# Optimization experiments

Measured on AMD Instinct MI355X. Metric: run time of the kernel, lower is better.

## Reference

```python
import jax, jax.numpy as jnp
import numpy as np
from jax import lax

N, CIN, H, W = 32, 128, 64, 64
COUT, KH, KW = 256, 3, 3
STRIDE = (1, 1)
PADDING = ((1, 1), (1, 1))


def setup_inputs() -> dict:
    key = jax.random.key(0)
    k1, k2, k3, k4 = jax.random.split(key, 4)
    # binary input in {0,1}
    x = jax.random.randint(k1, (N, CIN, H, W), 0, 2).astype(jnp.float32)
    # ternary weight in {-1,0,1}
    weight = (jax.random.randint(k2, (COUT, CIN, KH, KW), 0, 3) - 1).astype(jnp.float32)
    # integer bias (folded from BN, floored to int per get_sign_bias_from_bn)
    bias = jax.random.randint(k3, (COUT,), -200, 200).astype(jnp.float32)
    # sign in {-1,+1}, broadcast shape (1, COUT, 1, 1)
    sign = jnp.where(jax.random.bernoulli(k4, 0.5, (1, COUT, 1, 1)), 1.0, -1.0).astype(jnp.float32)
    return {"x": x, "weight": weight, "bias": bias, "sign": sign}


def reference(x, weight, bias, sign):
    # y = conv2d(x, W) + bias  (stride 1, pad 1, NCHW)
    y = lax.conv_general_dilated(
        x, weight,
        window_strides=STRIDE,
        padding=PADDING,
        dimension_numbers=("NCHW", "OIHW", "NCHW"),
    ) + bias[None, :, None, None]
    # rounding=True -> torch.round_(y)
    y = jnp.round(y)
    # output = 1 iff sign * y >= 0, cast back to input dtype
    return jnp.where(y * sign >= 0, jnp.float32(1), jnp.float32(0)).astype(x.dtype)
```

## Files before the change

### kernel.cpp

```cpp
#include <hip/hip_runtime.h>
#include <cstdint>


#define NIMG 32
#define CIN  128
#define HH   64
#define WW   64
#define COUT 256
#define X4ROW   4224
#define STG_SY  4352
#define STG_BYTES (4 * STG_SY)
#define LDS_TOTAL (STG_BYTES + 4 * X4ROW)
#define WQ4_BYTES ((size_t)9 * 8 * 2 * 64 * 16)

typedef int   v4i  __attribute__((ext_vector_type(4)));
typedef int   v8i  __attribute__((ext_vector_type(8)));
typedef float v16f __attribute__((ext_vector_type(16)));

__global__ __launch_bounds__(256) void w_prepack(const float* __restrict__ w,
                                                 int8_t* __restrict__ wq4) {
    const int idx = blockIdx.x * 256 + threadIdx.x;
    if (idx >= (int)WQ4_BYTES) return;
    const int b    = idx & 15;
    const int lane = (idx >> 4) & 63;
    const int s    = (idx >> 10) & 1;
    const int co32 = (idx >> 11) & 7;
    const int tap  = idx >> 14;
    const int co   = co32 * 32 + (lane & 31);
    const int ci0  = s * 64 + (lane >> 5) * 32 + b * 2;
    const int i0 = (int)w[(size_t)(co * CIN + ci0) * 9 + tap];
    const int i1 = (int)w[(size_t)(co * CIN + ci0 + 1) * 9 + tap];
    const uint32_t n0 = (i0 == 0) ? 0u : ((i0 > 0) ? 0x2u : 0xAu);
    const uint32_t n1 = (i1 == 0) ? 0u : ((i1 > 0) ? 0x2u : 0xAu);
    wq4[idx] = (int8_t)(n0 | (n1 << 4));
}

__device__ __forceinline__ v8i widen(v4i x) {
    v8i r = {x[0], x[1], x[2], x[3], 0, 0, 0, 0};
    return r;
}

__global__ __launch_bounds__(512) void binconv_fused(
    const float* __restrict__ x, const int8_t* __restrict__ wq4,
    const float* __restrict__ bias, const float* __restrict__ sign,
    float* __restrict__ out) {

    __shared__ __align__(16) int8_t Smem[LDS_TOTAL];
    int8_t* Stg = Smem;
    int8_t* X4  = Smem + STG_BYTES;

    const int t  = threadIdx.x;
    const int bx = blockIdx.x;
    const int n  = bx >> 5;
    const int y0 = (bx & 31) << 1;

    if (t < 256) {
        const int sy = t >> 6;
        const int pr = t & 63;
        const int y  = y0 + sy - 1;
        uint32_t* sp = (uint32_t*)(Stg + sy * STG_SY + pr * 68);
        if (y >= 0 && y < HH) {
            const uint4* r0 =
                (const uint4*)(x + (((size_t)n * CIN + 2 * pr)     * HH + y) * WW);
            const uint4* r1 =
                (const uint4*)(x + (((size_t)n * CIN + 2 * pr + 1) * HH + y) * WW);
#pragma unroll
            for (int q = 0; q < 16; ++q) {
                const uint4 a = r0[q], b = r1[q];
                uint32_t wd = ((a.x >> 28) & 0x2u)        | ((b.x >> 24) & 0x20u)
                            | ((a.y >> 20) & 0x200u)      | ((b.y >> 16) & 0x2000u)
                            | ((a.z >> 12) & 0x20000u)    | ((b.z >> 8) & 0x200000u)
                            | ((a.w >> 4)  & 0x2000000u)  | ( b.w       & 0x20000000u);
                sp[q] = wd;
            }
        } else {
#pragma unroll
            for (int q = 0; q < 16; ++q) sp[q] = 0u;
        }
    }
    __syncthreads();

    if (t < 264) {
        const int sy  = t / 66;
        const int pxp = t - sy * 66;
        int8_t* dst = X4 + sy * X4ROW + pxp * 64;
        if (pxp == 0 || pxp == 65) {
            const int4 z = {0, 0, 0, 0};
#pragma unroll
            for (int c = 0; c < 4; ++c) *(int4*)(dst + c * 16) = z;
        } else {
            const int8_t* src = Stg + sy * STG_SY + (pxp - 1);
            uint32_t wrd[16];
#pragma unroll
            for (int k = 0; k < 16; ++k) {
                const uint32_t b0 = (uint8_t)src[(4 * k + 0) * 68];
                const uint32_t b1 = (uint8_t)src[(4 * k + 1) * 68];
                const uint32_t b2 = (uint8_t)src[(4 * k + 2) * 68];
                const uint32_t b3 = (uint8_t)src[(4 * k + 3) * 68];
                wrd[k] = b0 | (b1 << 8) | (b2 << 16) | (b3 << 24);
            }
            const int sk = pxp & 3;
#pragma unroll
            for (int c = 0; c < 4; ++c) {
                int4 vv = {(int)wrd[c*4], (int)wrd[c*4+1],
                           (int)wrd[c*4+2], (int)wrd[c*4+3]};
                *(int4*)(dst + ((c ^ sk) << 4)) = vv;
            }
        }
    }
    __syncthreads();

    const int wid  = t >> 6;
    const int lane = t & 63;
    const int m_lo = lane & 31;
    const int hi   = lane >> 5;
    const int co_off = (wid >> 1) * 64;
    const int yw     = wid & 1;
    const int ct0    = co_off >> 5;

    const int8_t* Xw  = X4 + yw * X4ROW;
    const int8_t* wqb = wq4 + lane * 16;

    v16f acc[2][2] = {};

#pragma unroll
    for (int tap = 0; tap < 9; ++tap) {
        const int ky = tap / 3, kx = tap % 3;
        const int8_t* xl = Xw + ky * X4ROW;
        const int px0 = m_lo + kx;
        const int pk  = px0 & 3;

        v4i af[2][2];
#pragma unroll
        for (int c = 0; c < 2; ++c)
#pragma unroll
            for (int s = 0; s < 2; ++s)
                af[c][s] = *(const v4i*)(wqb
                    + ((((tap * 8 + ct0 + c) * 2) + s) << 10));

        v4i bf[2][2];
#pragma unroll
        for (int s = 0; s < 2; ++s) {
            const int sw = (((s << 1) + hi) ^ pk) << 4;
#pragma unroll
            for (int m = 0; m < 2; ++m)
                bf[m][s] = *(const v4i*)(xl + (px0 + m * 32) * 64 + sw);
        }
#pragma unroll
        for (int s = 0; s < 2; ++s)
#pragma unroll
            for (int c = 0; c < 2; ++c)
#pragma unroll
                for (int m = 0; m < 2; ++m)
                    acc[c][m] = __builtin_amdgcn_mfma_scale_f32_32x32x64_f8f6f4(
                        widen(af[c][s]), widen(bf[m][s]), acc[c][m],
                        4, 4,
                        0, 0x7F7F7F7F,
                        0, 0x7F7F7F7F);
    }

    const float* bco = bias + co_off;
    const float* sco = sign + co_off;
    float* outb = out + ((size_t)n * COUT + co_off) * (HH * WW)
                + (y0 + yw) * WW + m_lo;
#pragma unroll
    for (int c = 0; c < 2; ++c) {
#pragma unroll
        for (int r = 0; r < 16; ++r) {
            const int co_l = c * 32 + (r & 3) + 8 * (r >> 2) + 4 * hi;
            const float bv = bco[co_l];
            const float sv = sco[co_l];
            float* orow = outb + (size_t)co_l * (HH * WW);
#pragma unroll
            for (int m = 0; m < 2; ++m) {
                const float yv = acc[c][m][r] + bv;
                const bool on = (sv > 0.0f) ? (yv >= 0.0f) : (yv <= 0.0f);
                __builtin_nontemporal_store(on ? 1.0f : 0.0f, orow + m * 32);
            }
        }
    }
}

__global__ __launch_bounds__(256) void naive_conv(
    const float* __restrict__ x, const float* __restrict__ w,
    const float* __restrict__ bias, const float* __restrict__ sign,
    float* __restrict__ out) {
    const int idx = blockIdx.x * 256 + threadIdx.x;
    const int xc = idx & 63, y = (idx >> 6) & 63, co = (idx >> 12) & 255,
              n = idx >> 20;
    float s = 0.f;
    for (int ci = 0; ci < CIN; ++ci)
        for (int ky = 0; ky < 3; ++ky) {
            const int iy = y + ky - 1;
            if (iy < 0 || iy >= HH) continue;
            for (int kx = 0; kx < 3; ++kx) {
                const int ix = xc + kx - 1;
                if (ix < 0 || ix >= WW) continue;
                s += x[((size_t)(n * CIN + ci) * HH + iy) * WW + ix] *
                     w[((size_t)(co * CIN + ci) * 3 + ky) * 3 + kx];
            }
        }
    const float yv = s + bias[co];
    out[idx] = ((sign[co] > 0.f) ? (yv >= 0.f) : (yv <= 0.f)) ? 1.0f : 0.0f;
}

extern "C" void kernel_launch(void* const* d_in, const int* in_sizes, int n_in,
                              void* d_out, int out_size, void* d_ws, size_t ws_size,
                              hipStream_t stream) {
    const float* x    = (const float*)d_in[0];
    const float* w    = (const float*)d_in[1];
    const float* bias = (const float*)d_in[2];
    const float* sign = (const float*)d_in[3];
    float* out = (float*)d_out;

    if (ws_size < WQ4_BYTES) {
        naive_conv<<<dim3((NIMG * COUT * HH * WW) / 256), 256, 0, stream>>>(
            x, w, bias, sign, out);
        return;
    }
    int8_t* wq4 = (int8_t*)d_ws;

    w_prepack<<<dim3((int)((WQ4_BYTES + 255) / 256)), 256, 0, stream>>>(w, wq4);
    binconv_fused<<<dim3(NIMG * (HH / 2)), 512, 0, stream>>>(
        x, wq4, bias, sign, out);
}
```

Before: 206.2 us.

## Spread input staging over all threads, byte-transpose via perm, swizzle block order

The global-load stage now uses all 512 threads, each handling half a row, instead of 256 threads each doing a full row. The LDS byte transpose into the swizzled X4 layout now reads 32-bit words and uses v_perm byte shuffles instead of per-byte LDS reads, with a separate set of threads zeroing the pad columns. Block indices are remapped so that consecutive blocks interleave across images, which may change L2 locality and scheduling. The aim is to cut prologue latency in LDS and VALU before the MFMA loop. The risk is that the perm selectors or the 17-word stride indexing are wrong.

```diff
diff --git a/kernel.cpp b/kernel.cpp
--- a/kernel.cpp
+++ b/kernel.cpp
@@ -49,23 +49,25 @@
     int8_t* Stg = Smem;
     int8_t* X4  = Smem + STG_BYTES;
 
-    const int t  = threadIdx.x;
-    const int bx = blockIdx.x;
+    const int t      = threadIdx.x;
+    const int bx_raw = blockIdx.x;
+    const int bx = ((bx_raw & 7) << 7) | (bx_raw >> 3);
     const int n  = bx >> 5;
     const int y0 = (bx & 31) << 1;
 
-    if (t < 256) {
-        const int sy = t >> 6;
-        const int pr = t & 63;
+    {
+        const int sy = t >> 7;
+        const int pr = (t >> 1) & 63;
+        const int qh = t & 1;
         const int y  = y0 + sy - 1;
-        uint32_t* sp = (uint32_t*)(Stg + sy * STG_SY + pr * 68);
+        uint32_t* sp = (uint32_t*)(Stg + sy * STG_SY + pr * 68) + qh * 8;
         if (y >= 0 && y < HH) {
             const uint4* r0 =
-                (const uint4*)(x + (((size_t)n * CIN + 2 * pr)     * HH + y) * WW);
+                (const uint4*)(x + (((size_t)n * CIN + 2 * pr)     * HH + y) * WW) + qh * 8;
             const uint4* r1 =
-                (const uint4*)(x + (((size_t)n * CIN + 2 * pr + 1) * HH + y) * WW);
-#pragma unroll
-            for (int q = 0; q < 16; ++q) {
+                (const uint4*)(x + (((size_t)n * CIN + 2 * pr + 1) * HH + y) * WW) + qh * 8;
+#pragma unroll
+            for (int q = 0; q < 8; ++q) {
                 const uint4 a = r0[q], b = r1[q];
                 uint32_t wd = ((a.x >> 28) & 0x2u)        | ((b.x >> 24) & 0x20u)
                             | ((a.y >> 20) & 0x200u)      | ((b.y >> 16) & 0x2000u)
@@ -75,37 +77,50 @@
             }
         } else {
 #pragma unroll
-            for (int q = 0; q < 16; ++q) sp[q] = 0u;
+            for (int q = 0; q < 8; ++q) sp[q] = 0u;
         }
     }
     __syncthreads();
 
-    if (t < 264) {
-        const int sy  = t / 66;
-        const int pxp = t - sy * 66;
-        int8_t* dst = X4 + sy * X4ROW + pxp * 64;
-        if (pxp == 0 || pxp == 65) {
-            const int4 z = {0, 0, 0, 0};
-#pragma unroll
-            for (int c = 0; c < 4; ++c) *(int4*)(dst + c * 16) = z;
+    if (t < 288) {
+        if (t < 256) {
+            const int c    = t & 3;
+            const int pq   = (t >> 2) & 15;
+            const int sy   = t >> 6;
+            const int pxp0 = 1 + 4 * pq;
+            const uint32_t* srow = (const uint32_t*)(Stg + sy * STG_SY);
+            v4i val[4];
+#pragma unroll
+            for (int u = 0; u < 4; ++u) {
+                const int r0 = 16 * c + 4 * u;
+                const uint32_t S0 = srow[(r0 + 0) * 17 + pq];
+                const uint32_t S1 = srow[(r0 + 1) * 17 + pq];
+                const uint32_t S2 = srow[(r0 + 2) * 17 + pq];
+                const uint32_t S3 = srow[(r0 + 3) * 17 + pq];
+                const uint32_t M0 = __builtin_amdgcn_perm(S0, S1, 0x01050004u);
+                const uint32_t M1 = __builtin_amdgcn_perm(S0, S1, 0x03070206u);
+                const uint32_t M2 = __builtin_amdgcn_perm(S2, S3, 0x01050004u);
+                const uint32_t M3 = __builtin_amdgcn_perm(S2, S3, 0x03070206u);
+                const uint32_t X0 = __builtin_amdgcn_perm(M2, M0, 0x05040100u);
+                const uint32_t X1 = __builtin_amdgcn_perm(M2, M0, 0x07060302u);
+                const uint32_t X2 = __builtin_amdgcn_perm(M3, M1, 0x05040100u);
+                const uint32_t X3 = __builtin_amdgcn_perm(M3, M1, 0x07060302u);
+                val[0][u] = (int)X0; val[1][u] = (int)X1;
+                val[2][u] = (int)X2; val[3][u] = (int)X3;
+            }
+            int8_t* dsty = X4 + sy * X4ROW;
+#pragma unroll
+            for (int p = 0; p < 4; ++p) {
+                const int pxp = pxp0 + p;
+                *(v4i*)(dsty + pxp * 64 + ((c ^ (pxp & 3)) << 4)) = val[p];
+            }
         } else {
-            const int8_t* src = Stg + sy * STG_SY + (pxp - 1);
-            uint32_t wrd[16];
-#pragma unroll
-            for (int k = 0; k < 16; ++k) {
-                const uint32_t b0 = (uint8_t)src[(4 * k + 0) * 68];
-                const uint32_t b1 = (uint8_t)src[(4 * k + 1) * 68];
-                const uint32_t b2 = (uint8_t)src[(4 * k + 2) * 68];
-                const uint32_t b3 = (uint8_t)src[(4 * k + 3) * 68];
-                wrd[k] = b0 | (b1 << 8) | (b2 << 16) | (b3 << 24);
-            }
-            const int sk = pxp & 3;
-#pragma unroll
-            for (int c = 0; c < 4; ++c) {
-                int4 vv = {(int)wrd[c*4], (int)wrd[c*4+1],
-                           (int)wrd[c*4+2], (int)wrd[c*4+3]};
-                *(int4*)(dst + ((c ^ sk) << 4)) = vv;
-            }
+            const int u2   = t - 256;
+            const int c    = u2 & 3;
+            const int side = (u2 >> 2) & 1;
+            const int sy   = u2 >> 3;
+            const v4i z = {0, 0, 0, 0};
+            *(v4i*)(X4 + sy * X4ROW + (side ? 65 : 0) * 64 + (c << 4)) = z;
         }
     }
     __syncthreads();
```

Measured after the change: 210.5 us. 1.02x slower.
